# Optimization experiments

Hardware: AMD Instinct MI355X
Metric: run time of the kernel (lower is better)

## Reference

```python
import jax, jax.numpy as jnp
import numpy as np

TOKENS = 8192
IN_F = 4096
OUT_F = 16384
QMAX = 256  # uint8-style affine range [0, 255]


def setup_inputs() -> dict:
    key = jax.random.key(0)
    kx, kw, kb = jax.random.split(key, 3)
    x = jax.random.normal(kx, (TOKENS, IN_F), dtype=jnp.float32)
    weight_q = jax.random.randint(kw, (OUT_F, IN_F), 0, QMAX, dtype=jnp.int32)
    bias = jax.random.normal(kb, (OUT_F,), dtype=jnp.float32)
    scale = jnp.float32(0.01)   # per-tensor affine scale
    zero_point = 128            # per-tensor affine zero point (int constant)
    return {"x": x, "weight_q": weight_q, "bias": bias, "scale": scale, "zero_point": zero_point}


def reference(x, weight_q, bias, scale, zero_point):
    # Dequantize weight: (q - zero_point) -> fp32, then dense matmul.
    # out[t, o] = (sum_i x[t, i] * (wq[o, i] - zp)) * scale + bias[o]
    w_deq = (weight_q - zero_point).astype(jnp.float32)  # [out, in]
    acc = jnp.einsum('ti,oi->to', x, w_deq)              # [tokens, out]
    return acc * scale + bias
```

## Files before the change

kernel.cpp:

```cpp
#include <hip/hip_runtime.h>
#include <hip/hip_bf16.h>
#include <stdint.h>

#define M_DIM 8192
#define N_DIM 16384
#define K_DIM 4096

typedef short short8 __attribute__((ext_vector_type(8)));
typedef float floatx4 __attribute__((ext_vector_type(4)));
typedef int i32x4 __attribute__((ext_vector_type(4)));

__device__ __forceinline__ unsigned short f2bf(float f) {
    union { float f; unsigned u; } a;
    a.f = f;
    unsigned r = a.u + 0x7FFFu + ((a.u >> 16) & 1u);
    return (unsigned short)(r >> 16);
}

#define GLDS16(g, l)                                                     \
    __builtin_amdgcn_global_load_lds(                                    \
        (const __attribute__((address_space(1))) void*)(g),              \
        (__attribute__((address_space(3))) void*)(l), 16, 0, 0)

#define SBAR() asm volatile("s_barrier" ::: "memory")
#define WAIT_VM0() asm volatile("s_waitcnt vmcnt(0)" ::: "memory")
#define WAIT_VM8() asm volatile("s_waitcnt vmcnt(8)" ::: "memory")
#define SCHEDB() __builtin_amdgcn_sched_barrier(0)

__global__ __launch_bounds__(256)
void quant_x_kernel(const float4* __restrict__ x, int* __restrict__ xq,
                    float* __restrict__ sx) {
    const int row = blockIdx.x;
    const int t = threadIdx.x;
    const float4* px = x + (size_t)row * (K_DIM / 4);
    float4 v[4];
    float am = 0.f;
#pragma unroll
    for (int j = 0; j < 4; ++j) {
        v[j] = px[t + j * 256];
        am = fmaxf(am, fmaxf(fmaxf(fabsf(v[j].x), fabsf(v[j].y)),
                             fmaxf(fabsf(v[j].z), fabsf(v[j].w))));
    }
#pragma unroll
    for (int m = 32; m; m >>= 1) am = fmaxf(am, __shfl_xor(am, m));
    __shared__ float red[4];
    if ((t & 63) == 0) red[t >> 6] = am;
    __syncthreads();
    am = fmaxf(fmaxf(red[0], red[1]), fmaxf(red[2], red[3]));
    const float inv = am > 0.f ? 127.f / am : 0.f;
    if (t == 0) sx[row] = am * (1.f / 127.f);
    int* xo = xq + (size_t)row * (K_DIM / 4);
#pragma unroll
    for (int j = 0; j < 4; ++j) {
        int q0 = (int)rintf(v[j].x * inv);
        int q1 = (int)rintf(v[j].y * inv);
        int q2 = (int)rintf(v[j].z * inv);
        int q3 = (int)rintf(v[j].w * inv);
        xo[t + j * 256] = (q0 & 255) | ((q1 & 255) << 8) |
                          ((q2 & 255) << 16) | ((q3 & 255) << 24);
    }
}

__global__ void cvt_w8_kernel(const int4* __restrict__ w, int4* __restrict__ out,
                              const int* __restrict__ zp_p, int n16) {
    const int zp = *zp_p;
    int idx = blockIdx.x * blockDim.x + threadIdx.x;
    int stride = gridDim.x * blockDim.x;
    for (int i = idx; i < n16; i += stride) {
        int4 r;
        int* rp = (int*)&r;
#pragma unroll
        for (int j = 0; j < 4; ++j) {
            int4 q = w[i * 4 + j];
            rp[j] = ((q.x - zp) & 255) | (((q.y - zp) & 255) << 8) |
                    (((q.z - zp) & 255) << 16) | (((q.w - zp) & 255) << 24);
        }
        out[i] = r;
    }
}


#define LOAD_AR(BUF, MH, AF)                                               \
    do {                                                                   \
        const char* p_ = smem + (BUF)*65536 + (MH)*16384 + wm*8192;        \
        _Pragma("unroll") for (int mf = 0; mf < 4; ++mf) {                 \
            AF[mf][0] = *(const i32x4*)(p_ + mf*2048 + laneK0);            \
            AF[mf][1] = *(const i32x4*)(p_ + mf*2048 + laneK1);            \
        }                                                                  \
    } while (0)

#define LOAD_BR(BUF, NH, BF)                                               \
    do {                                                                   \
        const char* p_ = smem + (BUF)*65536 + 32768 + (NH)*16384 + wn*4096;\
        _Pragma("unroll") for (int nf = 0; nf < 2; ++nf) {                 \
            BF[nf][0] = *(const i32x4*)(p_ + nf*2048 + laneK0);            \
            BF[nf][1] = *(const i32x4*)(p_ + nf*2048 + laneK1);            \
        }                                                                  \
    } while (0)

#define STAGE_A0(BUF)                                                      \
    do {                                                                   \
        GLDS16(pA00, smem + (BUF)*65536 + st16); pA00 += 128;              \
        GLDS16(pA01, smem + (BUF)*65536 + 8192 + st16); pA01 += 128;       \
    } while (0)
#define STAGE_A1(BUF)                                                      \
    do {                                                                   \
        GLDS16(pA10, smem + (BUF)*65536 + 16384 + st16); pA10 += 128;      \
        GLDS16(pA11, smem + (BUF)*65536 + 16384 + 8192 + st16); pA11 += 128;\
    } while (0)
#define STAGE_B0(BUF)                                                      \
    do {                                                                   \
        GLDS16(pB00, smem + (BUF)*65536 + 32768 + st16); pB00 += 128;      \
        GLDS16(pB01, smem + (BUF)*65536 + 32768 + 8192 + st16); pB01 += 128;\
    } while (0)
#define STAGE_B1(BUF)                                                      \
    do {                                                                   \
        GLDS16(pB10, smem + (BUF)*65536 + 49152 + st16); pB10 += 128;      \
        GLDS16(pB11, smem + (BUF)*65536 + 49152 + 8192 + st16); pB11 += 128;\
    } while (0)

#define MFMA_Q(AF, BF, MH, NH)                                             \
    do {                                                                   \
        __builtin_amdgcn_s_setprio(1);                                     \
        _Pragma("unroll") for (int kk = 0; kk < 2; ++kk)                   \
        _Pragma("unroll") for (int mf = 0; mf < 4; ++mf)                   \
        _Pragma("unroll") for (int nf = 0; nf < 2; ++nf)                   \
            acc[(MH)*4+mf][(NH)*2+nf] =                                    \
                __builtin_amdgcn_mfma_i32_16x16x64_i8(                     \
                    AF[mf][kk], BF[nf][kk], acc[(MH)*4+mf][(NH)*2+nf],     \
                    0, 0, 0);                                              \
        __builtin_amdgcn_s_setprio(0);                                     \
    } while (0)

#define BODY(B, SMODE)                                                     \
    do {                                                                   \
        if ((SMODE) == 0) { WAIT_VM0(); } else { WAIT_VM8(); }             \
        SBAR();                                                            \
        LOAD_AR(B, 0, aF);                                                 \
        LOAD_BR(B, 0, bF0);                                                \
        LOAD_BR(B, 1, bF1);                                                \
        MFMA_Q(aF, bF0, 0, 0);                                             \
        MFMA_Q(aF, bF1, 0, 1);                                             \
        SCHEDB();                                                          \
        LOAD_AR(B, 1, aF);                                                 \
        MFMA_Q(aF, bF1, 1, 1);                                             \
        MFMA_Q(aF, bF0, 1, 0);                                             \
        SBAR();                                                            \
        if ((SMODE) == 2) {                                                \
            STAGE_A0(B); STAGE_B0(B); STAGE_B1(B); STAGE_A1(B);            \
        }                                                                  \
    } while (0)

__global__ __launch_bounds__(512, 2)
void gemm8i_kernel(const int8_t* __restrict__ Aq, const int8_t* __restrict__ Bq,
                   const float* __restrict__ bias,
                   const float* __restrict__ scale_p,
                   const float* __restrict__ sx,
                   float* __restrict__ out) {
    __shared__ __align__(16) char smem[131072];

    const int t = threadIdx.x;
    const int lane = t & 63;
    const int wid = t >> 6;
    const int wm = wid >> 2;
    const int wn = wid & 3;

    int bid = blockIdx.x;
    int sz = (bid & 7) * 256 + (bid >> 3);
    const int bx = sz & 63;
    const int by = sz >> 6;
    const int brow = by << 8;
    const int bcol = bx << 8;

    const int laneK0 = (lane & 15) * 128 + (((lane >> 4) * 16) ^ ((lane & 7) << 4));
    const int laneK1 = (lane & 15) * 128 + ((((lane >> 4) * 16) + 64) ^ ((lane & 7) << 4));

    size_t aoffs[2], boffs[2];
#pragma unroll
    for (int g = 0; g < 2; ++g) {
        unsigned u = g * 8192 + t * 16;
        unsigned up = u ^ (((u >> 7) & 7) << 4);
        aoffs[g] = (size_t)(brow + ((up >> 13) & 1) * 128 + ((up >> 7) & 63)) * K_DIM
                   + (up & 127);
        boffs[g] = (size_t)(bcol + ((up >> 12) & 3) * 64 + ((up >> 7) & 31)) * K_DIM
                   + (up & 127);
    }
    const int8_t* pA00 = Aq + aoffs[0];
    const int8_t* pA01 = Aq + aoffs[1];
    const int8_t* pA10 = Aq + aoffs[0] + 262144;
    const int8_t* pA11 = Aq + aoffs[1] + 262144;
    const int8_t* pB00 = Bq + boffs[0];
    const int8_t* pB01 = Bq + boffs[1];
    const int8_t* pB10 = Bq + boffs[0] + 131072;
    const int8_t* pB11 = Bq + boffs[1] + 131072;
    const int st16 = t * 16;

    i32x4 acc[8][4] = {};
    i32x4 aF[4][2], bF0[2][2], bF1[2][2];

    const int NT = K_DIM / 128;

    STAGE_A0(0); STAGE_B0(0); STAGE_B1(0); STAGE_A1(0);
    STAGE_A0(1); STAGE_B0(1); STAGE_B1(1); STAGE_A1(1);

    for (int it = 0; it < (NT - 2) / 2; ++it) {
        BODY(0, 2);
        BODY(1, 2);
    }
    BODY(0, 1);
    BODY(1, 0);

    const float scale = *scale_p;
    const int crow0 = brow + wm * 128 + ((lane >> 4) << 2);
    const int ccol0 = bcol + wn * 64 + (lane & 15);
    float bv[4];
#pragma unroll
    for (int nf = 0; nf < 4; ++nf) bv[nf] = bias[ccol0 + nf * 16];
#pragma unroll
    for (int mf = 0; mf < 8; ++mf) {
#pragma unroll
        for (int j = 0; j < 4; ++j) {
            const int r = crow0 + mf * 16 + j;
            const float s2 = scale * sx[r];
            float* orow = out + (size_t)r * N_DIM;
#pragma unroll
            for (int nf = 0; nf < 4; ++nf)
                orow[ccol0 + nf * 16] = (float)acc[mf][nf][j] * s2 + bv[nf];
        }
    }
}

__global__ __launch_bounds__(256)
void gemm_fb_kernel(const float* __restrict__ Xf, const int* __restrict__ Wq,
                    const float* __restrict__ bias,
                    const float* __restrict__ scale_p,
                    const int* __restrict__ zp_p,
                    float* __restrict__ out) {
    const int NB = N_DIM / 128;
    int nwg = gridDim.x;
    int cpx = nwg >> 3;
    int bid = blockIdx.x;
    int swz = (bid & 7) * cpx + (bid >> 3);
    int bx = swz % NB;
    int by = swz / NB;
    const int brow = by * 128;
    const int bcol = bx * 128;

    __shared__ __align__(16) ushort sA[128 * 32];
    __shared__ __align__(16) ushort sB[128 * 32];

    const int t = threadIdx.x;
    const int lane = t & 63;
    const int wid = t >> 6;
    const int wr = wid >> 1;
    const int wc = wid & 1;

    floatx4 acc[4][4] = {};

    const int xr = t >> 1;
    const int xc = (t & 1) << 4;
    const int zp = *zp_p;

    const int arow = wr * 64 + (lane & 15);
    const int acol = (lane >> 4) << 3;
    const int brow_f = wc * 64 + (lane & 15);

    for (int k0 = 0; k0 < K_DIM; k0 += 32) {
        __syncthreads();
        const float* gx = Xf + (size_t)(brow + xr) * K_DIM + k0 + xc;
        ushort* dA = &sA[xr * 32 + xc];
#pragma unroll
        for (int i = 0; i < 4; ++i) {
            float4 v = ((const float4*)gx)[i];
            ushort4 u;
            u.x = f2bf(v.x); u.y = f2bf(v.y); u.z = f2bf(v.z); u.w = f2bf(v.w);
            *(ushort4*)(dA + i * 4) = u;
        }
        const int* gw = Wq + (size_t)(bcol + xr) * K_DIM + k0 + xc;
        ushort* dB = &sB[xr * 32 + xc];
#pragma unroll
        for (int i = 0; i < 4; ++i) {
            int4 q = ((const int4*)gw)[i];
            ushort4 u;
            u.x = f2bf((float)(q.x - zp));
            u.y = f2bf((float)(q.y - zp));
            u.z = f2bf((float)(q.z - zp));
            u.w = f2bf((float)(q.w - zp));
            *(ushort4*)(dB + i * 4) = u;
        }
        __syncthreads();

        short8 af[4], bfr[4];
#pragma unroll
        for (int m = 0; m < 4; ++m)
            af[m] = *(const short8*)&sA[(arow + m * 16) * 32 + acol];
#pragma unroll
        for (int n = 0; n < 4; ++n)
            bfr[n] = *(const short8*)&sB[(brow_f + n * 16) * 32 + acol];

#pragma unroll
        for (int m = 0; m < 4; ++m)
#pragma unroll
            for (int n = 0; n < 4; ++n)
                acc[m][n] = __builtin_amdgcn_mfma_f32_16x16x32_bf16(
                    af[m], bfr[n], acc[m][n], 0, 0, 0);
    }

    const float scale = *scale_p;
    const int colbase = bcol + wc * 64 + (lane & 15);
    const int rowbase = brow + wr * 64 + ((lane >> 4) << 2);
    float bv[4];
#pragma unroll
    for (int n = 0; n < 4; ++n) bv[n] = bias[colbase + n * 16];
#pragma unroll
    for (int m = 0; m < 4; ++m) {
        const int r0 = rowbase + m * 16;
#pragma unroll
        for (int j = 0; j < 4; ++j) {
            float* orow = out + (size_t)(r0 + j) * N_DIM;
#pragma unroll
            for (int n = 0; n < 4; ++n)
                orow[colbase + n * 16] = acc[m][n][j] * scale + bv[n];
        }
    }
}

extern "C" void kernel_launch(void* const* d_in, const int* in_sizes, int n_in,
                              void* d_out, int out_size, void* d_ws, size_t ws_size,
                              hipStream_t stream) {
    const float* x = (const float*)d_in[0];
    const int* wq = (const int*)d_in[1];
    const float* bias = (const float*)d_in[2];
    const float* scale = (const float*)d_in[3];
    const int* zp = (const int*)d_in[4];
    float* out = (float*)d_out;

    const size_t xq_bytes = (size_t)M_DIM * K_DIM;
    const size_t wb_bytes = (size_t)N_DIM * K_DIM;
    const size_t sx_bytes = (size_t)M_DIM * 4;

    if (ws_size >= xq_bytes + wb_bytes + sx_bytes) {
        int8_t* xq = (int8_t*)d_ws;
        int8_t* wb = (int8_t*)d_ws + xq_bytes;
        float* sx = (float*)((char*)d_ws + xq_bytes + wb_bytes);
        quant_x_kernel<<<M_DIM, 256, 0, stream>>>((const float4*)x, (int*)xq, sx);
        cvt_w8_kernel<<<2048, 256, 0, stream>>>((const int4*)wq, (int4*)wb, zp,
                                                (N_DIM * K_DIM) / 16);
        const int nblocks = (M_DIM / 256) * (N_DIM / 256);
        gemm8i_kernel<<<nblocks, 512, 0, stream>>>(xq, wb, bias, scale, sx, out);
    } else {
        const int nblocks = (M_DIM / 128) * (N_DIM / 128);
        gemm_fb_kernel<<<nblocks, 256, 0, stream>>>(x, wq, bias, scale, zp, out);
    }
}
```

Before: 692.6 us.

## Load A operand fragments directly from global into registers, bypassing LDS

```diff
diff --git a/kernel.cpp b/kernel.cpp
--- a/kernel.cpp
+++ b/kernel.cpp
@@ -25,6 +25,8 @@
 #define SBAR() asm volatile("s_barrier" ::: "memory")
 #define WAIT_VM0() asm volatile("s_waitcnt vmcnt(0)" ::: "memory")
 #define WAIT_VM8() asm volatile("s_waitcnt vmcnt(8)" ::: "memory")
+#define WAIT_VM12() asm volatile("s_waitcnt vmcnt(12)" ::: "memory")
+#define WAIT_VM20() asm volatile("s_waitcnt vmcnt(20)" ::: "memory")
 #define SCHEDB() __builtin_amdgcn_sched_barrier(0)
 
 __global__ __launch_bounds__(256)
@@ -80,44 +82,36 @@
 }
 
 
-#define LOAD_AR(BUF, MH, AF)                                               \
-    do {                                                                   \
-        const char* p_ = smem + (BUF)*65536 + (MH)*16384 + wm*8192;        \
-        _Pragma("unroll") for (int mf = 0; mf < 4; ++mf) {                 \
-            AF[mf][0] = *(const i32x4*)(p_ + mf*2048 + laneK0);            \
-            AF[mf][1] = *(const i32x4*)(p_ + mf*2048 + laneK1);            \
-        }                                                                  \
-    } while (0)
-
 #define LOAD_BR(BUF, NH, BF)                                               \
     do {                                                                   \
-        const char* p_ = smem + (BUF)*65536 + 32768 + (NH)*16384 + wn*4096;\
+        const char* p_ = smem + (BUF)*32768 + (NH)*16384 + wn*4096;        \
         _Pragma("unroll") for (int nf = 0; nf < 2; ++nf) {                 \
             BF[nf][0] = *(const i32x4*)(p_ + nf*2048 + laneK0);            \
             BF[nf][1] = *(const i32x4*)(p_ + nf*2048 + laneK1);            \
         }                                                                  \
     } while (0)
 
-#define STAGE_A0(BUF)                                                      \
-    do {                                                                   \
-        GLDS16(pA00, smem + (BUF)*65536 + st16); pA00 += 128;              \
-        GLDS16(pA01, smem + (BUF)*65536 + 8192 + st16); pA01 += 128;       \
-    } while (0)
-#define STAGE_A1(BUF)                                                      \
-    do {                                                                   \
-        GLDS16(pA10, smem + (BUF)*65536 + 16384 + st16); pA10 += 128;      \
-        GLDS16(pA11, smem + (BUF)*65536 + 16384 + 8192 + st16); pA11 += 128;\
-    } while (0)
 #define STAGE_B0(BUF)                                                      \
     do {                                                                   \
-        GLDS16(pB00, smem + (BUF)*65536 + 32768 + st16); pB00 += 128;      \
-        GLDS16(pB01, smem + (BUF)*65536 + 32768 + 8192 + st16); pB01 += 128;\
+        GLDS16(pB00, smem + (BUF)*32768 + st16); pB00 += 128;              \
+        GLDS16(pB01, smem + (BUF)*32768 + 8192 + st16); pB01 += 128;       \
     } while (0)
 #define STAGE_B1(BUF)                                                      \
     do {                                                                   \
-        GLDS16(pB10, smem + (BUF)*65536 + 49152 + st16); pB10 += 128;      \
-        GLDS16(pB11, smem + (BUF)*65536 + 49152 + 8192 + st16); pB11 += 128;\
-    } while (0)
+        GLDS16(pB10, smem + (BUF)*32768 + 16384 + st16); pB10 += 128;      \
+        GLDS16(pB11, smem + (BUF)*32768 + 16384 + 8192 + st16); pB11 += 128;\
+    } while (0)
+
+#define LOAD_A_HALF(H)                                                     \
+    do {                                                                   \
+        _Pragma("unroll") for (int mf = 0; mf < 4; ++mf) {                 \
+            aF[mf][0] = *(const i32x4*)(Aq + aoff[mf] + (H) * 262144u);    \
+            aF[mf][1] = *(const i32x4*)(Aq + aoff[mf] + (H) * 262144u + 64);\
+        }                                                                  \
+    } while (0)
+
+#define ADV_A()                                                            \
+    do { _Pragma("unroll") for (int mf = 0; mf < 4; ++mf) aoff[mf] += 128; } while (0)
 
 #define MFMA_Q(AF, BF, MH, NH)                                             \
     do {                                                                   \
@@ -134,21 +128,20 @@
 
 #define BODY(B, SMODE)                                                     \
     do {                                                                   \
-        if ((SMODE) == 0) { WAIT_VM0(); } else { WAIT_VM8(); }             \
+        if ((SMODE) == 0) { WAIT_VM8(); } else { WAIT_VM20(); }            \
         SBAR();                                                            \
-        LOAD_AR(B, 0, aF);                                                 \
         LOAD_BR(B, 0, bF0);                                                \
         LOAD_BR(B, 1, bF1);                                                \
-        MFMA_Q(aF, bF0, 0, 0);                                             \
+        MFMA_Q(aF, bF0, 0, 0);    \
         MFMA_Q(aF, bF1, 0, 1);                                             \
         SCHEDB();                                                          \
-        LOAD_AR(B, 1, aF);                                                 \
+        LOAD_A_HALF(1);          \
         MFMA_Q(aF, bF1, 1, 1);                                             \
         MFMA_Q(aF, bF0, 1, 0);                                             \
+        SCHEDB();                                                          \
+        if ((SMODE) >= 1) { ADV_A(); LOAD_A_HALF(0); }    \
         SBAR();                                                            \
-        if ((SMODE) == 2) {                                                \
-            STAGE_A0(B); STAGE_B0(B); STAGE_B1(B); STAGE_A1(B);            \
-        }                                                                  \
+        if ((SMODE) == 2) { STAGE_B0(B); STAGE_B1(B); }                    \
     } while (0)
 
 __global__ __launch_bounds__(512, 2)
@@ -157,7 +150,7 @@
                    const float* __restrict__ scale_p,
                    const float* __restrict__ sx,
                    float* __restrict__ out) {
-    __shared__ __align__(16) char smem[131072];
+    __shared__ __align__(16) char smem[65536];
 
     const int t = threadIdx.x;
     const int lane = t & 63;
@@ -175,33 +168,36 @@
     const int laneK0 = (lane & 15) * 128 + (((lane >> 4) * 16) ^ ((lane & 7) << 4));
     const int laneK1 = (lane & 15) * 128 + ((((lane >> 4) * 16) + 64) ^ ((lane & 7) << 4));
 
-    size_t aoffs[2], boffs[2];
+    size_t boffs[2];
 #pragma unroll
     for (int g = 0; g < 2; ++g) {
         unsigned u = g * 8192 + t * 16;
         unsigned up = u ^ (((u >> 7) & 7) << 4);
-        aoffs[g] = (size_t)(brow + ((up >> 13) & 1) * 128 + ((up >> 7) & 63)) * K_DIM
-                   + (up & 127);
         boffs[g] = (size_t)(bcol + ((up >> 12) & 3) * 64 + ((up >> 7) & 31)) * K_DIM
                    + (up & 127);
     }
-    const int8_t* pA00 = Aq + aoffs[0];
-    const int8_t* pA01 = Aq + aoffs[1];
-    const int8_t* pA10 = Aq + aoffs[0] + 262144;
-    const int8_t* pA11 = Aq + aoffs[1] + 262144;
     const int8_t* pB00 = Bq + boffs[0];
     const int8_t* pB01 = Bq + boffs[1];
     const int8_t* pB10 = Bq + boffs[0] + 131072;
     const int8_t* pB11 = Bq + boffs[1] + 131072;
     const int st16 = t * 16;
 
+    unsigned aoff[4];
+#pragma unroll
+    for (int mf = 0; mf < 4; ++mf) {
+        const int r0 = brow + wm * 128 + mf * 16 + (lane & 15);
+        aoff[mf] = (unsigned)r0 * K_DIM + ((lane >> 4) << 4);
+    }
+
     i32x4 acc[8][4] = {};
     i32x4 aF[4][2], bF0[2][2], bF1[2][2];
 
     const int NT = K_DIM / 128;
 
-    STAGE_A0(0); STAGE_B0(0); STAGE_B1(0); STAGE_A1(0);
-    STAGE_A0(1); STAGE_B0(1); STAGE_B1(1); STAGE_A1(1);
+    STAGE_B0(0); STAGE_B1(0);
+    STAGE_B0(1); STAGE_B1(1);
+    LOAD_A_HALF(0);
+    WAIT_VM12();
 
     for (int it = 0; it < (NT - 2) / 2; ++it) {
         BODY(0, 2);
```

After: 1.278 ms. 1.85x slower.
